# Optimization experiments

Measured on AMD Instinct MI355X. Metric: run time of the kernel, lower is better.

The kernel has to match this reference:

```python
import jax, jax.numpy as jnp
import numpy as np

BS, N, IN_DIM, OUT_DIM = 16, 2048, 32, 64
CHEB_K, E_NODE, T_D = 3, 10, 8
EMBED = E_NODE + T_D  # 18, matches weights_pool dim 0
TOPK = 10


def setup_inputs() -> dict:
    key = jax.random.key(0)
    ks = jax.random.split(key, 7)
    return {
        "x": jax.random.normal(ks[0], (BS, N, IN_DIM), jnp.float32),
        "node_emb": jax.random.normal(ks[1], (N, E_NODE), jnp.float32),
        "t": jax.random.normal(ks[2], (BS, T_D), jnp.float32),
        "n_t": jax.random.normal(ks[3], (BS, T_D), jnp.float32),
        "p": jax.random.normal(ks[4], (BS, 1, 1), jnp.float32),
        "weights_pool": jax.random.normal(ks[5], (EMBED, CHEB_K, IN_DIM, OUT_DIM), jnp.float32) * 0.1,
        "bias_pool": jax.random.normal(ks[6], (EMBED, OUT_DIM), jnp.float32) * 0.1,
    }


def reference(x, node_emb, t, n_t, p, weights_pool, bias_pool):
    bs, n, _ = x.shape
    # static adjacency from node embeddings, broadcast over batch: [bs, N, N]
    a = (node_emb @ node_emb.T)[None, :, :]
    # temporal scalar correction: bmm([bs,1,td],[bs,td,1]) -> [bs,1,1]
    a_t = jnp.einsum('bd,bd->b', n_t, t)[:, None, None]
    _a = a + a_t
    # period branch: scaled relu adjacency, then dynamic topK sparsify
    pre = jax.nn.relu((1.0 + 0.3 * jax.nn.sigmoid(p)) * _a)  # [bs, N, N]
    # topK tie-break noise (torch.rand_like * 0.01); deterministic key here
    noise = jax.random.uniform(jax.random.key(42), pre.shape, jnp.float32) * 0.01
    _, idx = jax.lax.top_k(pre + noise, TOPK)  # idx: [bs, N, TOPK]
    mask = jnp.zeros_like(pre).at[
        jnp.arange(bs)[:, None, None], jnp.arange(n)[None, :, None], idx
    ].set(1.0)
    # masked entries stay 0 (not -inf) before softmax, as in the original
    A = jax.nn.softmax(pre * mask, axis=2)
    # Chebyshev polynomial supports: T0=I, T1=A, Tk = 2*A@T(k-1) - T(k-2)
    I = jnp.broadcast_to(jnp.eye(n, dtype=x.dtype), (bs, n, n))
    supports = [I, A]
    for _ in range(2, CHEB_K):
        supports.append(2.0 * (A @ supports[-1]) - supports[-2])
    S = jnp.stack(supports, axis=1)  # [bs, K, N, N]
    # node-adaptive embedding: cat(node_emb, n_t) -> [bs, N, EMBED]
    ne = jnp.concatenate(
        [jnp.broadcast_to(node_emb[None], (bs, n, E_NODE)),
         jnp.broadcast_to(n_t[:, None, :], (bs, n, T_D))], axis=-1)
    # graph conv features: [bs, N, K, in]
    x_g = jnp.einsum('bknm,bmc->bnkc', S, x)
    bias = ne @ bias_pool  # [bs, N, out]
    # fused per-node dynamic-weight contraction:
    # original: W = einsum(bnd,dkio->bnkio); out = einsum(bnki,bnkio->bno)
    out = jnp.einsum('bnki,bnd,dkio->bno', x_g, ne, weights_pool) + bias
    return out
```

## Files before the change

### kernel.cpp

```cpp
#include <hip/hip_runtime.h>
#include <hip/hip_bf16.h>


constexpr int BS = 16, NN_ = 2048, CIN = 32, OUT = 64, TK = 10;
constexpr int ROWS = BS * NN_;

__device__ __forceinline__ void tf2x32(unsigned x0, unsigned x1,
                                       unsigned& o0, unsigned& o1) {
  const unsigned k0 = 0u, k1 = 42u;
  const unsigned ks2 = k0 ^ k1 ^ 0x1BD11BDAu;
#define TF_R(rot) { x0 += x1; x1 = (x1 << rot) | (x1 >> (32 - rot)); x1 ^= x0; }
  x0 += k0; x1 += k1;
  TF_R(13) TF_R(15) TF_R(26) TF_R(6)
  x0 += k1; x1 += ks2 + 1u;
  TF_R(17) TF_R(29) TF_R(16) TF_R(24)
  x0 += ks2; x1 += k0 + 2u;
  TF_R(13) TF_R(15) TF_R(26) TF_R(6)
  x0 += k0; x1 += k1 + 3u;
  TF_R(17) TF_R(29) TF_R(16) TF_R(24)
  x0 += k1; x1 += ks2 + 4u;
  TF_R(13) TF_R(15) TF_R(26) TF_R(6)
  x0 += ks2; x1 += k0 + 5u;
#undef TF_R
  o0 = x0; o1 = x1;
}

__device__ __forceinline__ float noise_val(unsigned flat) {
  unsigned o0, o1; tf2x32(0u, flat, o0, o1);
  unsigned bits = o0 ^ o1;
  float u = __uint_as_float((bits >> 9) | 0x3f800000u) - 1.0f;
  return 0.01f * u;
}

__global__ __launch_bounds__(256) void k_pre(const float* __restrict__ ne,
                                             const float* __restrict__ n_t,
                                             const float* __restrict__ wp,
                                             const float* __restrict__ x,
                                             float* __restrict__ Wn,
                                             float* __restrict__ Wt,
                                             double* __restrict__ partX,
                                             float* __restrict__ csy_part) {
  const int bid = blockIdx.x;
  __shared__ float neS[16][10];
  __shared__ double red[8][32];

  if (bid < 768) {
    const int ng = bid / 6, sg = bid % 6;
    const int slot = sg * 256 + threadIdx.x;
    const int ki = slot >> 4, o4 = slot & 15;

    if (threadIdx.x < 160)
      neS[threadIdx.x / 10][threadIdx.x % 10] =
          ne[(ng * 16 + threadIdx.x / 10) * 10 + threadIdx.x % 10];

    const float4* wp4 = (const float4*)wp;
    float4 w[10];
    #pragma unroll
    for (int d = 0; d < 10; ++d) w[d] = wp4[(d * 96 + ki) * 16 + o4];
    __syncthreads();

    float4* Wn4 = (float4*)Wn;
    #pragma unroll 4
    for (int nn = 0; nn < 16; ++nn) {
      float4 acc = {0.f, 0.f, 0.f, 0.f};
      #pragma unroll
      for (int d = 0; d < 10; ++d) {
        float e = neS[nn][d];
        acc.x = fmaf(e, w[d].x, acc.x); acc.y = fmaf(e, w[d].y, acc.y);
        acc.z = fmaf(e, w[d].z, acc.z); acc.w = fmaf(e, w[d].w, acc.w);
      }
      Wn4[((size_t)(ng * 16 + nn) * 96 + ki) * 16 + o4] = acc;
    }
  } else if (bid < 864) {
    int gid = (bid - 768) * 256 + threadIdx.x;
    int b = gid / 1536, rem = gid % 1536, ki = rem >> 4, o4 = rem & 15;
    const float4* wp4 = (const float4*)wp;
    float4 acc = {0.f, 0.f, 0.f, 0.f};
    #pragma unroll
    for (int d = 0; d < 8; ++d) {
      float e = n_t[b * 8 + d];
      float4 w = wp4[((10 + d) * 96 + ki) * 16 + o4];
      acc.x = fmaf(e, w.x, acc.x); acc.y = fmaf(e, w.y, acc.y);
      acc.z = fmaf(e, w.z, acc.z); acc.w = fmaf(e, w.w, acc.w);
    }
    ((float4*)Wt)[(b * 96 + ki) * 16 + o4] = acc;
  } else if (bid < 1120) {
    const int bb = bid - 864;
    const int b = bb >> 4, ch = bb & 15;
    const int c = threadIdx.x & 31, g = threadIdx.x >> 5;
    double acc = 0.0;
    for (int m = ch * 128 + g; m < ch * 128 + 128; m += 8)
      acc += (double)x[(((b << 11) + m) << 5) + c];
    red[g][c] = acc;
    __syncthreads();
    if (g == 0) {
      double s2 = red[0][c];
      #pragma unroll
      for (int i = 1; i < 8; ++i) s2 += red[i][c];
      partX[(((b << 4) + ch) << 5) + c] = s2;
    }
  } else {
    #pragma unroll
    for (int i = 0; i < 16; ++i) csy_part[i * 256 + threadIdx.x] = 0.f;
  }
}

__global__ __launch_bounds__(256, 4) void k_topk(const float* __restrict__ ne,
                                                 const float* __restrict__ t,
                                                 const float* __restrict__ n_t,
                                                 const float* __restrict__ p,
                                                 const float* __restrict__ x,
                                                 const double* __restrict__ partX,
                                                 float* __restrict__ cinv,
                                                 int* __restrict__ idxb,
                                                 float* __restrict__ wgt,
                                                 float* __restrict__ Y1,
                                                 float* __restrict__ csy_part) {
  const int n = blockIdx.x;
  const int warp = threadIdx.x >> 6, lane = threadIdx.x & 63;

  __shared__ float rowS[2048];
  __shared__ float neN[10];
  __shared__ float candA[128];
  __shared__ int   candM[128];
  __shared__ int   Cs;
  __shared__ unsigned long long keyS[4][128];
  __shared__ int   winI[16][10];
  __shared__ float winW[16][10];
  __shared__ float ciS[16];
  __shared__ float csL[512];

  if (threadIdx.x < 10) neN[threadIdx.x] = ne[n * 10 + threadIdx.x];
  __syncthreads();

  {
    float ner[10];
    #pragma unroll
    for (int d = 0; d < 10; ++d) ner[d] = neN[d];
    #pragma unroll
    for (int g2 = 0; g2 < 2; ++g2) {
      const int m0 = g2 * 1024 + threadIdx.x * 4;
      const float4* nf = (const float4*)(ne + (size_t)m0 * 10);
      float acc4[4] = {0.f, 0.f, 0.f, 0.f};
      #pragma unroll
      for (int i = 0; i < 10; ++i) {
        float4 q = nf[i];
        #pragma unroll
        for (int j = 0; j < 4; ++j) {
          const int e = i * 4 + j;
          const int rr = e / 10, d = e % 10;
          acc4[rr] = fmaf(ner[d], (&q.x)[j], acc4[rr]);
        }
      }
      *(float4*)&rowS[m0] = make_float4(acc4[0], acc4[1], acc4[2], acc4[3]);
    }
  }
  __syncthreads();

  if (warp == 0) {
    float lm = -3.4e38f;
    #pragma unroll
    for (int j = 0; j < 8; ++j) {
      float4 f = ((const float4*)rowS)[j * 64 + lane];
      lm = fmaxf(lm, fmaxf(fmaxf(f.x, f.y), fmaxf(f.z, f.w)));
    }
    float last = 3.4e38f;
    for (int rd = 0; rd < 11; ++rd) {
      float x2 = (lm < last) ? lm : -3.4e38f;
      #pragma unroll
      for (int off = 32; off > 0; off >>= 1) x2 = fmaxf(x2, __shfl_xor(x2, off));
      last = x2;
    }
    const float T = last - 0.0101f;

    int cnt = 0;
    #pragma unroll
    for (int slot = 0; slot < 32; ++slot) {
      float v = rowS[(slot >> 2) * 256 + lane * 4 + (slot & 3)];
      bool c = (v >= T);
      unsigned long long mk = __ballot(c);
      if (c) {
        int pos = cnt + __popcll(mk & ((1ull << lane) - 1ull));
        if (pos < 128) {
          candA[pos] = v;
          candM[pos] = ((slot >> 2) << 8) + (lane << 2) + (slot & 3);
        }
      }
      cnt += (int)__popcll(mk);
    }
    if (lane == 0) Cs = cnt < 128 ? cnt : 128;
  } else {
    for (int e = threadIdx.x - 64; e < 512; e += 192) {
      double s2 = 0.0;
      #pragma unroll
      for (int ch = 0; ch < 16; ++ch)
        s2 += partX[((((e >> 5) << 4) + ch) << 5) + (e & 31)];
      csL[e] = (float)s2;
    }
  }
  __syncthreads();

  const int C = Cs;
  const bool two = (C > 64);
  float a0c = 0.f, a1c = 0.f; int m0c = 0, m1c = 0;
  if (lane < C) { a0c = candA[lane]; m0c = candM[lane]; }
  if (two && lane + 64 < C) { a1c = candA[lane + 64]; m1c = candM[lane + 64]; }

  for (int bi = 0; bi < 4; ++bi) {
    const int b = warp * 4 + bi;
    const int r = (b << 11) | n;

    float at = 0.f;
    #pragma unroll
    for (int d = 0; d < 8; ++d) at = fmaf(n_t[b * 8 + d], t[b * 8 + d], at);
    const float s = 1.0f + 0.3f * (1.0f / (1.0f + expf(-p[b])));

    float pre0 = fmaxf(s * (a0c + at), 0.f);
    unsigned long long k0 = 0ull;
    if (lane < C) {
      float key0 = pre0 + noise_val((unsigned)r * 2048u + (unsigned)m0c);
      k0 = ((unsigned long long)__float_as_uint(key0) << 32) |
           (unsigned)(2047 - m0c);
      keyS[warp][lane] = k0;
    }
    float pre1 = 0.f;
    unsigned long long k1 = 0ull;
    if (two) {
      if (lane + 64 < C) {
        pre1 = fmaxf(s * (a1c + at), 0.f);
        float key1 = pre1 + noise_val((unsigned)r * 2048u + (unsigned)m1c);
        k1 = ((unsigned long long)__float_as_uint(key1) << 32) |
             (unsigned)(2047 - m1c);
      }
      keyS[warp][lane + 64] = k1;
    }

    int rank0 = 0, rank1 = 0;
    for (int j2 = 0; j2 < C; ++j2) {
      unsigned long long kj = keyS[warp][j2];
      rank0 += (kj > k0) ? 1 : 0;
      if (two) rank1 += (kj > k1) ? 1 : 0;
    }
    bool w0 = (lane < C) && (rank0 < 10);
    bool w1 = two && (lane + 64 < C) && (rank1 < 10);

    float e0 = w0 ? expf(pre0) : 0.f;
    float e1 = w1 ? expf(pre1) : 0.f;
    float sum = e0 + e1;
    #pragma unroll
    for (int off = 32; off > 0; off >>= 1) sum += __shfl_xor(sum, off);
    const float ci = 1.0f / (2038.0f + sum);

    unsigned long long mk0 = __ballot(w0);
    if (w0) {
      int pos = __popcll(mk0 & ((1ull << lane) - 1ull));
      idxb[r * 10 + pos] = m0c;
      wgt[r * 10 + pos] = (e0 - 1.0f) * ci;
      winI[b][pos] = m0c;
      winW[b][pos] = (e0 - 1.0f) * ci;
    }
    if (two) {
      unsigned long long mk1 = __ballot(w1);
      int base = __popcll(mk0);
      if (w1) {
        int pos = base + __popcll(mk1 & ((1ull << lane) - 1ull));
        idxb[r * 10 + pos] = m1c;
        wgt[r * 10 + pos] = (e1 - 1.0f) * ci;
        winI[b][pos] = m1c;
        winW[b][pos] = (e1 - 1.0f) * ci;
      }
    }
    if (lane == 0) { cinv[r] = ci; ciS[b] = ci; }
  }

  #pragma unroll
  for (int pass = 0; pass < 2; ++pass) {
    const int bi2 = pass * 2 + (lane >> 5);
    const int b = warp * 4 + bi2;
    const int c = lane & 31;
    const int r = (b << 11) | n;
    float acc = ciS[b] * csL[(b << 5) + c];
    #pragma unroll
    for (int j = 0; j < 10; ++j) {
      int m = winI[b][j];
      float w = winW[b][j];
      acc = fmaf(w, x[(((b << 11) + m) << 5) + c], acc);
    }
    Y1[(size_t)r * 32 + c] = acc;
    atomicAdd(&csy_part[((n & 7) << 9) + (b << 5) + c], acc);
  }
}

__global__ __launch_bounds__(256) void k_v(const float* __restrict__ x,
                                           const float* __restrict__ Y1,
                                           const float* __restrict__ cinv,
                                           const int* __restrict__ idxb,
                                           const float* __restrict__ wgt,
                                           const float* __restrict__ csy_part,
                                           float* __restrict__ V) {
  int gid = blockIdx.x * 256 + threadIdx.x;
  int r = gid >> 5, c = gid & 31, b = r >> 11;
  float cs = 0.f;
  #pragma unroll
  for (int k = 0; k < 8; ++k) cs += csy_part[(k << 9) + (b << 5) + c];
  float y2 = cinv[r] * cs;
  #pragma unroll
  for (int j = 0; j < 10; ++j)
    y2 = fmaf(wgt[r * 10 + j], Y1[(((b << 11) + idxb[r * 10 + j]) << 5) + c], y2);
  float xv = x[gid], y1v = Y1[gid];
  V[r * 96 + c] = xv;
  V[r * 96 + 32 + c] = y1v;
  V[r * 96 + 64 + c] = 2.f * y2 - xv;
}

__global__ __launch_bounds__(256) void k_outn(const float* __restrict__ ne,
                                              const float* __restrict__ n_t,
                                              const float* __restrict__ Wn,
                                              const float* __restrict__ bp,
                                              const float* __restrict__ V,
                                              float* __restrict__ out) {
  const int n = blockIdx.x;
  __shared__ float Vs[16][100];
  __shared__ float bNs[64];

  for (int e = threadIdx.x; e < 384; e += 256) {
    int b = e / 24, j4 = e % 24;
    float4 f = *(const float4*)&V[((size_t)(b << 11) + n) * 96 + j4 * 4];
    *(float4*)&Vs[b][j4 * 4] = f;
  }
  if (threadIdx.x < 64) {
    float acc = 0.f;
    #pragma unroll
    for (int d = 0; d < 10; ++d)
      acc = fmaf(ne[n * 10 + d], bp[d * 64 + threadIdx.x], acc);
    bNs[threadIdx.x] = acc;
  }
  __syncthreads();

  const int b = threadIdx.x >> 4, og = threadIdx.x & 15;
  const float4* Wr = (const float4*)(Wn + (size_t)n * 6144);

  float4 acc = {0.f, 0.f, 0.f, 0.f};
  #pragma unroll 4
  for (int ki = 0; ki < 96; ++ki) {
    float4 wv = Wr[ki * 16 + og];
    float v = Vs[b][ki];
    acc.x = fmaf(v, wv.x, acc.x); acc.y = fmaf(v, wv.y, acc.y);
    acc.z = fmaf(v, wv.z, acc.z); acc.w = fmaf(v, wv.w, acc.w);
  }

  float4 res;
  #pragma unroll
  for (int q = 0; q < 4; ++q) {
    int o = og * 4 + q;
    float bT = 0.f;
    #pragma unroll
    for (int d = 0; d < 8; ++d)
      bT = fmaf(n_t[b * 8 + d], bp[(10 + d) * 64 + o], bT);
    (&res.x)[q] = (&acc.x)[q] + bNs[o] + bT;
  }
  *(float4*)&out[((size_t)(b << 11) + n) * 64 + og * 4] = res;
}

__global__ __launch_bounds__(512) void k_outt(const float* __restrict__ WtG,
                                              const float* __restrict__ V,
                                              float* __restrict__ out) {
  const int b = blockIdx.x >> 5, tile = blockIdx.x & 31;
  __shared__ float Wt[96][64];
  {
    const float4* src = (const float4*)(WtG + (size_t)b * 6144);
    float4* dst = (float4*)Wt;
    for (int e = threadIdx.x; e < 1536; e += 512) dst[e] = src[e];
  }
  __syncthreads();
  const int wave = threadIdx.x >> 6, lane = threadIdx.x & 63;
  const int og = lane & 15, rg = lane >> 4;
  const int r0 = tile * 64 + wave * 8 + rg * 2;

  float acc[2][4] = {};
  for (int ki4 = 0; ki4 < 24; ++ki4) {
    float4 vv[2];
    #pragma unroll
    for (int i = 0; i < 2; ++i)
      vv[i] = *(const float4*)&V[(size_t)((b << 11) + r0 + i) * 96 + ki4 * 4];
    #pragma unroll
    for (int t2 = 0; t2 < 4; ++t2) {
      float4 wv = *(const float4*)&Wt[ki4 * 4 + t2][og * 4];
      #pragma unroll
      for (int i = 0; i < 2; ++i) {
        float vi = (t2 == 0) ? vv[i].x : (t2 == 1) ? vv[i].y
                 : (t2 == 2) ? vv[i].z : vv[i].w;
        acc[i][0] = fmaf(vi, wv.x, acc[i][0]);
        acc[i][1] = fmaf(vi, wv.y, acc[i][1]);
        acc[i][2] = fmaf(vi, wv.z, acc[i][2]);
        acc[i][3] = fmaf(vi, wv.w, acc[i][3]);
      }
    }
  }
  #pragma unroll
  for (int i = 0; i < 2; ++i) {
    size_t oidx = (size_t)((b << 11) + r0 + i) * 64 + og * 4;
    float4 cur = *(float4*)&out[oidx];
    cur.x += acc[i][0]; cur.y += acc[i][1];
    cur.z += acc[i][2]; cur.w += acc[i][3];
    *(float4*)&out[oidx] = cur;
  }
}

extern "C" void kernel_launch(void* const* d_in, const int* in_sizes, int n_in,
                              void* d_out, int out_size, void* d_ws, size_t ws_size,
                              hipStream_t stream) {
  const float* x   = (const float*)d_in[0];
  const float* ne  = (const float*)d_in[1];
  const float* t   = (const float*)d_in[2];
  const float* n_t = (const float*)d_in[3];
  const float* p   = (const float*)d_in[4];
  const float* wp  = (const float*)d_in[5];
  const float* bp  = (const float*)d_in[6];
  float* out = (float*)d_out;
  float* ws = (float*)d_ws;
  (void)in_sizes; (void)n_in; (void)out_size; (void)ws_size;

  float* cinv     = ws;
  int*   idxb     = (int*)(cinv + 32768);
  float* wgt      = (float*)(idxb + 327680);
  float* csy_part = wgt + 327680;
  double* partX   = (double*)(csy_part + 4096);
  float* Y1       = (float*)(partX + 8192);
  float* V        = Y1 + 1048576;
  float* Wt       = V + 3145728;
  float* Wn       = Wt + 98304;

  k_pre  <<<1121, 256, 0, stream>>>(ne, n_t, wp, x, Wn, Wt, partX, csy_part);
  k_topk <<<2048, 256, 0, stream>>>(ne, t, n_t, p, x, partX,
                                    cinv, idxb, wgt, Y1, csy_part);
  k_v    <<<4096, 256, 0, stream>>>(x, Y1, cinv, idxb, wgt, csy_part, V);
  k_outn <<<2048, 256, 0, stream>>>(ne, n_t, Wn, bp, V, out);
  k_outt <<<512, 512, 0, stream>>>(Wt, V, out);
}
```

Before: 179.6 us.

## Compute topk candidates in every warp and reduce column sums via atomics

Every warp now redundantly computes the row threshold and candidate list instead of warp 0 alone, which removes a block-wide barrier and the idle wait of the other warps. When there are at most 32 candidates, a new path handles two batches per warp in 32-lane halves. Column sums of x are accumulated with double atomics in k_pre instead of per-chunk partials that every topk block re-reduced, and a memset zeroes the accumulators in place of the extra zeroing block. The cost is redundant candidate-selection work in each warp and an added memset launch.

```diff
diff --git a/kernel.cpp b/kernel.cpp
--- a/kernel.cpp
+++ b/kernel.cpp
@@ -38,8 +38,7 @@
                                              const float* __restrict__ x,
                                              float* __restrict__ Wn,
                                              float* __restrict__ Wt,
-                                             double* __restrict__ partX,
-                                             float* __restrict__ csy_part) {
+                                             double* __restrict__ csxD) {
   const int bid = blockIdx.x;
   __shared__ float neS[16][10];
   __shared__ double red[8][32];
@@ -84,7 +83,7 @@
       acc.z = fmaf(e, w.z, acc.z); acc.w = fmaf(e, w.w, acc.w);
     }
     ((float4*)Wt)[(b * 96 + ki) * 16 + o4] = acc;
-  } else if (bid < 1120) {
+  } else {
     const int bb = bid - 864;
     const int b = bb >> 4, ch = bb & 15;
     const int c = threadIdx.x & 31, g = threadIdx.x >> 5;
@@ -97,11 +96,8 @@
       double s2 = red[0][c];
       #pragma unroll
       for (int i = 1; i < 8; ++i) s2 += red[i][c];
-      partX[(((b << 4) + ch) << 5) + c] = s2;
-    }
-  } else {
-    #pragma unroll
-    for (int i = 0; i < 16; ++i) csy_part[i * 256 + threadIdx.x] = 0.f;
+      atomicAdd(&csxD[(b << 5) + c], s2);
+    }
   }
 }
 
@@ -110,7 +106,7 @@
                                                  const float* __restrict__ n_t,
                                                  const float* __restrict__ p,
                                                  const float* __restrict__ x,
-                                                 const double* __restrict__ partX,
+                                                 const double* __restrict__ csxD,
                                                  float* __restrict__ cinv,
                                                  int* __restrict__ idxb,
                                                  float* __restrict__ wgt,
@@ -120,23 +116,17 @@
   const int warp = threadIdx.x >> 6, lane = threadIdx.x & 63;
 
   __shared__ float rowS[2048];
-  __shared__ float neN[10];
-  __shared__ float candA[128];
-  __shared__ int   candM[128];
-  __shared__ int   Cs;
+  __shared__ float candA[4][128];
+  __shared__ int   candM[4][128];
   __shared__ unsigned long long keyS[4][128];
   __shared__ int   winI[16][10];
   __shared__ float winW[16][10];
   __shared__ float ciS[16];
-  __shared__ float csL[512];
-
-  if (threadIdx.x < 10) neN[threadIdx.x] = ne[n * 10 + threadIdx.x];
-  __syncthreads();
 
   {
     float ner[10];
     #pragma unroll
-    for (int d = 0; d < 10; ++d) ner[d] = neN[d];
+    for (int d = 0; d < 10; ++d) ner[d] = ne[n * 10 + d];
     #pragma unroll
     for (int g2 = 0; g2 < 2; ++g2) {
       const int m0 = g2 * 1024 + threadIdx.x * 4;
@@ -157,120 +147,158 @@
   }
   __syncthreads();
 
-  if (warp == 0) {
-    float lm = -3.4e38f;
-    #pragma unroll
-    for (int j = 0; j < 8; ++j) {
-      float4 f = ((const float4*)rowS)[j * 64 + lane];
-      lm = fmaxf(lm, fmaxf(fmaxf(f.x, f.y), fmaxf(f.z, f.w)));
-    }
-    float last = 3.4e38f;
-    for (int rd = 0; rd < 11; ++rd) {
-      float x2 = (lm < last) ? lm : -3.4e38f;
-      #pragma unroll
-      for (int off = 32; off > 0; off >>= 1) x2 = fmaxf(x2, __shfl_xor(x2, off));
-      last = x2;
-    }
-    const float T = last - 0.0101f;
-
-    int cnt = 0;
-    #pragma unroll
-    for (int slot = 0; slot < 32; ++slot) {
-      float v = rowS[(slot >> 2) * 256 + lane * 4 + (slot & 3)];
-      bool c = (v >= T);
-      unsigned long long mk = __ballot(c);
-      if (c) {
-        int pos = cnt + __popcll(mk & ((1ull << lane) - 1ull));
-        if (pos < 128) {
-          candA[pos] = v;
-          candM[pos] = ((slot >> 2) << 8) + (lane << 2) + (slot & 3);
+  float lm = -3.4e38f;
+  #pragma unroll
+  for (int j = 0; j < 8; ++j) {
+    float4 f = ((const float4*)rowS)[j * 64 + lane];
+    lm = fmaxf(lm, fmaxf(fmaxf(f.x, f.y), fmaxf(f.z, f.w)));
+  }
+  float last = 3.4e38f;
+  for (int rd = 0; rd < 11; ++rd) {
+    float x2 = (lm < last) ? lm : -3.4e38f;
+    #pragma unroll
+    for (int off = 32; off > 0; off >>= 1) x2 = fmaxf(x2, __shfl_xor(x2, off));
+    last = x2;
+  }
+  const float T = last - 0.0101f;
+
+  int cnt = 0;
+  #pragma unroll
+  for (int slot = 0; slot < 32; ++slot) {
+    float v = rowS[(slot >> 2) * 256 + lane * 4 + (slot & 3)];
+    bool c = (v >= T);
+    unsigned long long mk = __ballot(c);
+    if (c) {
+      int pos = cnt + __popcll(mk & ((1ull << lane) - 1ull));
+      if (pos < 128) {
+        candA[warp][pos] = v;
+        candM[warp][pos] = ((slot >> 2) << 8) + (lane << 2) + (slot & 3);
+      }
+    }
+    cnt += (int)__popcll(mk);
+  }
+  const int C = cnt < 128 ? cnt : 128;
+
+  if (C <= 32) {
+    const int h = lane >> 5, j = lane & 31;
+    for (int pair = 0; pair < 2; ++pair) {
+      const int b = warp * 4 + pair * 2 + h;
+      const int r = (b << 11) | n;
+
+      float at = 0.f;
+      #pragma unroll
+      for (int d = 0; d < 8; ++d) at = fmaf(n_t[b * 8 + d], t[b * 8 + d], at);
+      const float s = 1.0f + 0.3f * (1.0f / (1.0f + expf(-p[b])));
+
+      const bool act = (j < C);
+      float pre = 0.f; int mj = 0;
+      unsigned long long kk = 0ull;
+      if (act) {
+        float aj = candA[warp][j]; mj = candM[warp][j];
+        pre = fmaxf(s * (aj + at), 0.f);
+        float key = pre + noise_val((unsigned)r * 2048u + (unsigned)mj);
+        kk = ((unsigned long long)__float_as_uint(key) << 32) |
+             (unsigned)(2047 - mj);
+      }
+      keyS[warp][lane] = kk;
+
+      int rank = 0;
+      for (int j2 = 0; j2 < C; ++j2) {
+        unsigned long long kj = keyS[warp][h * 32 + j2];
+        rank += (kj > kk) ? 1 : 0;
+      }
+      const bool win = act && (rank < 10);
+
+      float e = win ? expf(pre) : 0.f;
+      float sum = e;
+      #pragma unroll
+      for (int off = 16; off > 0; off >>= 1) sum += __shfl_xor(sum, off);
+      const float ci = 1.0f / (2038.0f + sum);
+
+      unsigned long long mask = __ballot(win);
+      unsigned mh = (unsigned)(mask >> (h * 32));
+      if (win) {
+        int pos = __popc(mh & ((1u << j) - 1u));
+        idxb[r * 10 + pos] = mj;
+        wgt[r * 10 + pos] = (e - 1.0f) * ci;
+        winI[b][pos] = mj;
+        winW[b][pos] = (e - 1.0f) * ci;
+      }
+      if (j == 0) { cinv[r] = ci; ciS[b] = ci; }
+    }
+  } else {
+    const bool two = (C > 64);
+    float a0c = 0.f, a1c = 0.f; int m0c = 0, m1c = 0;
+    if (lane < C) { a0c = candA[warp][lane]; m0c = candM[warp][lane]; }
+    if (two && lane + 64 < C) {
+      a1c = candA[warp][lane + 64]; m1c = candM[warp][lane + 64];
+    }
+    for (int bi = 0; bi < 4; ++bi) {
+      const int b = warp * 4 + bi;
+      const int r = (b << 11) | n;
+
+      float at = 0.f;
+      #pragma unroll
+      for (int d = 0; d < 8; ++d) at = fmaf(n_t[b * 8 + d], t[b * 8 + d], at);
+      const float s = 1.0f + 0.3f * (1.0f / (1.0f + expf(-p[b])));
+
+      float pre0 = fmaxf(s * (a0c + at), 0.f);
+      unsigned long long k0 = 0ull;
+      if (lane < C) {
+        float key0 = pre0 + noise_val((unsigned)r * 2048u + (unsigned)m0c);
+        k0 = ((unsigned long long)__float_as_uint(key0) << 32) |
+             (unsigned)(2047 - m0c);
+        keyS[warp][lane] = k0;
+      }
+      float pre1 = 0.f;
+      unsigned long long k1 = 0ull;
+      if (two) {
+        if (lane + 64 < C) {
+          pre1 = fmaxf(s * (a1c + at), 0.f);
+          float key1 = pre1 + noise_val((unsigned)r * 2048u + (unsigned)m1c);
+          k1 = ((unsigned long long)__float_as_uint(key1) << 32) |
+               (unsigned)(2047 - m1c);
         }
-      }
-      cnt += (int)__popcll(mk);
-    }
-    if (lane == 0) Cs = cnt < 128 ? cnt : 128;
-  } else {
-    for (int e = threadIdx.x - 64; e < 512; e += 192) {
-      double s2 = 0.0;
-      #pragma unroll
-      for (int ch = 0; ch < 16; ++ch)
-        s2 += partX[((((e >> 5) << 4) + ch) << 5) + (e & 31)];
-      csL[e] = (float)s2;
-    }
-  }
-  __syncthreads();
-
-  const int C = Cs;
-  const bool two = (C > 64);
-  float a0c = 0.f, a1c = 0.f; int m0c = 0, m1c = 0;
-  if (lane < C) { a0c = candA[lane]; m0c = candM[lane]; }
-  if (two && lane + 64 < C) { a1c = candA[lane + 64]; m1c = candM[lane + 64]; }
-
-  for (int bi = 0; bi < 4; ++bi) {
-    const int b = warp * 4 + bi;
-    const int r = (b << 11) | n;
-
-    float at = 0.f;
-    #pragma unroll
-    for (int d = 0; d < 8; ++d) at = fmaf(n_t[b * 8 + d], t[b * 8 + d], at);
-    const float s = 1.0f + 0.3f * (1.0f / (1.0f + expf(-p[b])));
-
-    float pre0 = fmaxf(s * (a0c + at), 0.f);
-    unsigned long long k0 = 0ull;
-    if (lane < C) {
-      float key0 = pre0 + noise_val((unsigned)r * 2048u + (unsigned)m0c);
-      k0 = ((unsigned long long)__float_as_uint(key0) << 32) |
-           (unsigned)(2047 - m0c);
-      keyS[warp][lane] = k0;
-    }
-    float pre1 = 0.f;
-    unsigned long long k1 = 0ull;
-    if (two) {
-      if (lane + 64 < C) {
-        pre1 = fmaxf(s * (a1c + at), 0.f);
-        float key1 = pre1 + noise_val((unsigned)r * 2048u + (unsigned)m1c);
-        k1 = ((unsigned long long)__float_as_uint(key1) << 32) |
-             (unsigned)(2047 - m1c);
-      }
-      keyS[warp][lane + 64] = k1;
-    }
-
-    int rank0 = 0, rank1 = 0;
-    for (int j2 = 0; j2 < C; ++j2) {
-      unsigned long long kj = keyS[warp][j2];
-      rank0 += (kj > k0) ? 1 : 0;
-      if (two) rank1 += (kj > k1) ? 1 : 0;
-    }
-    bool w0 = (lane < C) && (rank0 < 10);
-    bool w1 = two && (lane + 64 < C) && (rank1 < 10);
-
-    float e0 = w0 ? expf(pre0) : 0.f;
-    float e1 = w1 ? expf(pre1) : 0.f;
-    float sum = e0 + e1;
-    #pragma unroll
-    for (int off = 32; off > 0; off >>= 1) sum += __shfl_xor(sum, off);
-    const float ci = 1.0f / (2038.0f + sum);
-
-    unsigned long long mk0 = __ballot(w0);
-    if (w0) {
-      int pos = __popcll(mk0 & ((1ull << lane) - 1ull));
-      idxb[r * 10 + pos] = m0c;
-      wgt[r * 10 + pos] = (e0 - 1.0f) * ci;
-      winI[b][pos] = m0c;
-      winW[b][pos] = (e0 - 1.0f) * ci;
-    }
-    if (two) {
-      unsigned long long mk1 = __ballot(w1);
-      int base = __popcll(mk0);
-      if (w1) {
-        int pos = base + __popcll(mk1 & ((1ull << lane) - 1ull));
-        idxb[r * 10 + pos] = m1c;
-        wgt[r * 10 + pos] = (e1 - 1.0f) * ci;
-        winI[b][pos] = m1c;
-        winW[b][pos] = (e1 - 1.0f) * ci;
-      }
-    }
-    if (lane == 0) { cinv[r] = ci; ciS[b] = ci; }
+        keyS[warp][lane + 64] = k1;
+      }
+
+      int rank0 = 0, rank1 = 0;
+      for (int j2 = 0; j2 < C; ++j2) {
+        unsigned long long kj = keyS[warp][j2];
+        rank0 += (kj > k0) ? 1 : 0;
+        if (two) rank1 += (kj > k1) ? 1 : 0;
+      }
+      bool w0 = (lane < C) && (rank0 < 10);
+      bool w1 = two && (lane + 64 < C) && (rank1 < 10);
+
+      float e0 = w0 ? expf(pre0) : 0.f;
+      float e1 = w1 ? expf(pre1) : 0.f;
+      float sum = e0 + e1;
+      #pragma unroll
+      for (int off = 32; off > 0; off >>= 1) sum += __shfl_xor(sum, off);
+      const float ci = 1.0f / (2038.0f + sum);
+
+      unsigned long long mk0 = __ballot(w0);
+      if (w0) {
+        int pos = __popcll(mk0 & ((1ull << lane) - 1ull));
+        idxb[r * 10 + pos] = m0c;
+        wgt[r * 10 + pos] = (e0 - 1.0f) * ci;
+        winI[b][pos] = m0c;
+        winW[b][pos] = (e0 - 1.0f) * ci;
+      }
+      if (two) {
+        unsigned long long mk1 = __ballot(w1);
+        int base = __popcll(mk0);
+        if (w1) {
+          int pos = base + __popcll(mk1 & ((1ull << lane) - 1ull));
+          idxb[r * 10 + pos] = m1c;
+          wgt[r * 10 + pos] = (e1 - 1.0f) * ci;
+          winI[b][pos] = m1c;
+          winW[b][pos] = (e1 - 1.0f) * ci;
+        }
+      }
+      if (lane == 0) { cinv[r] = ci; ciS[b] = ci; }
+    }
   }
 
   #pragma unroll
@@ -279,7 +307,7 @@
     const int b = warp * 4 + bi2;
     const int c = lane & 31;
     const int r = (b << 11) | n;
-    float acc = ciS[b] * csL[(b << 5) + c];
+    float acc = ciS[b] * (float)csxD[(b << 5) + c];
     #pragma unroll
     for (int j = 0; j < 10; ++j) {
       int m = winI[b][j];
@@ -424,15 +452,17 @@
   float* cinv     = ws;
   int*   idxb     = (int*)(cinv + 32768);
   float* wgt      = (float*)(idxb + 327680);
-  float* csy_part = wgt + 327680;
-  double* partX   = (double*)(csy_part + 4096);
-  float* Y1       = (float*)(partX + 8192);
+  double* csxD    = (double*)(wgt + 327680);
+  float* csy_part = (float*)(csxD + 512);
+  float* Y1       = csy_part + 4096;
   float* V        = Y1 + 1048576;
   float* Wt       = V + 3145728;
   float* Wn       = Wt + 98304;
 
-  k_pre  <<<1121, 256, 0, stream>>>(ne, n_t, wp, x, Wn, Wt, partX, csy_part);
-  k_topk <<<2048, 256, 0, stream>>>(ne, t, n_t, p, x, partX,
+  hipMemsetAsync(csxD, 0, 512 * 8 + 4096 * 4, stream);
+
+  k_pre  <<<1120, 256, 0, stream>>>(ne, n_t, wp, x, Wn, Wt, csxD);
+  k_topk <<<2048, 256, 0, stream>>>(ne, t, n_t, p, x, csxD,
                                     cinv, idxb, wgt, Y1, csy_part);
   k_v    <<<4096, 256, 0, stream>>>(x, Y1, cinv, idxb, wgt, csy_part, V);
   k_outn <<<2048, 256, 0, stream>>>(ne, n_t, Wn, bp, V, out);
```

New measurement: 173.8 us. 1.03x faster.
